# Kernel tuning notes

Hardware: AMD Instinct MI355X
Metric: run time of the kernel (lower is better)

Reference implementation:

```python
import jax, jax.numpy as jnp
import numpy as np

N, IN, H, C = 50000, 128, 256, 64
E_G, E_K = 600000, 800000
MLP_H = H // 2  # multiplier=2 (residual=False)
EPS = 1e-5


def _w(k, i, o):
    return (jax.random.normal(k, (i, o), jnp.float32) * np.float32(1.0 / np.sqrt(i)))


def setup_inputs() -> dict:
    key = jax.random.key(0)
    ks = jax.random.split(key, 32)
    inp = {
        "feat": jax.random.normal(ks[0], (N, IN), jnp.float32),
        "g_src": jax.random.randint(ks[1], (E_G,), 0, N, jnp.int32),
        "g_dst": jax.random.randint(ks[2], (E_G,), 0, N, jnp.int32),
        "k_src": jax.random.randint(ks[3], (E_K,), 0, N, jnp.int32),
        "k_dst": jax.random.randint(ks[4], (E_K,), 0, N, jnp.int32),
        # local GraphSAGE: 3 SAGEConv layers (IN->H, H->H, H->H)
        "lw_self_0": _w(ks[5], IN, H), "lw_neigh_0": _w(ks[6], IN, H), "lb_0": jnp.zeros((H,), jnp.float32),
        "lw_self_1": _w(ks[7], H, H),  "lw_neigh_1": _w(ks[8], H, H),  "lb_1": jnp.zeros((H,), jnp.float32),
        "lw_self_2": _w(ks[9], H, H),  "lw_neigh_2": _w(ks[10], H, H), "lb_2": jnp.zeros((H,), jnp.float32),
        # global GraphSAGE: 2 SAGEConv layers (IN->H, H->H)
        "gw_self_0": _w(ks[11], IN, H), "gw_neigh_0": _w(ks[12], IN, H), "gb_0": jnp.zeros((H,), jnp.float32),
        "gw_self_1": _w(ks[13], H, H),  "gw_neigh_1": _w(ks[14], H, H),  "gb_1": jnp.zeros((H,), jnp.float32),
        # MLP head: Linear(2H -> MLP_H), BatchNorm1d(MLP_H), ReLU, Linear(MLP_H -> C)
        "mlp_w1": _w(ks[15], 2 * H, MLP_H), "mlp_b1": jnp.zeros((MLP_H,), jnp.float32),
        "bn_gamma": jnp.ones((MLP_H,), jnp.float32), "bn_beta": jnp.zeros((MLP_H,), jnp.float32),
        "mlp_w2": _w(ks[16], MLP_H, C), "mlp_b2": jnp.zeros((C,), jnp.float32),
    }
    return inp


def sage_conv(src, dst, h, w_self, w_neigh, b):
    # DGL SAGEConv, mean aggregator: fc_self(h) + fc_neigh(mean_{u in N(v)} h_u) + bias
    msg = h[src]                                             # [E, d] irregular gather
    agg = jax.ops.segment_sum(msg, dst, num_segments=N)      # [N, d] irregular scatter-add
    deg = jax.ops.segment_sum(jnp.ones(src.shape, h.dtype), dst, num_segments=N)
    h_neigh = agg / jnp.maximum(deg, 1.0)[:, None]           # isolated nodes -> 0
    return h @ w_self + h_neigh @ w_neigh + b


def batch_norm(x, gamma, beta):
    mu = jnp.mean(x, axis=0)
    var = jnp.mean(jnp.square(x - mu), axis=0)  # biased var, as in torch BN forward
    return gamma * (x - mu) * jax.lax.rsqrt(var + EPS) + beta


def reference(feat, g_src, g_dst, k_src, k_dst,
              lw_self_0, lw_neigh_0, lb_0, lw_self_1, lw_neigh_1, lb_1,
              lw_self_2, lw_neigh_2, lb_2,
              gw_self_0, gw_neigh_0, gb_0, gw_self_1, gw_neigh_1, gb_1,
              mlp_w1, mlp_b1, bn_gamma, bn_beta, mlp_w2, mlp_b2):
    # local GraphSAGE (3 layers, relu between; dropout = identity in eval)
    h = feat
    h = jax.nn.relu(sage_conv(g_src, g_dst, h, lw_self_0, lw_neigh_0, lb_0))
    h = jax.nn.relu(sage_conv(g_src, g_dst, h, lw_self_1, lw_neigh_1, lb_1))
    local_emb = sage_conv(g_src, g_dst, h, lw_self_2, lw_neigh_2, lb_2)
    # global GraphSAGE on knn graph (2 layers)
    h = feat
    h = jax.nn.relu(sage_conv(k_src, k_dst, h, gw_self_0, gw_neigh_0, gb_0))
    global_emb = sage_conv(k_src, k_dst, h, gw_self_1, gw_neigh_1, gb_1)
    # fuse + BatchNorm-MLP head
    x = jnp.concatenate([local_emb, global_emb], axis=1)     # [N, 2H]
    x = x @ mlp_w1 + mlp_b1
    x = jax.nn.relu(batch_norm(x, bn_gamma, bn_beta))
    return x @ mlp_w2 + mlp_b2                               # [N, C]
```

## Files before the change

kernel.cpp:

```cpp
#include <hip/hip_runtime.h>

#define NN   50000
#define IN_F 128
#define HF   256
#define COUT 64
#define MLPH 128
#define EG   600000
#define EK   800000
#define RNG  6250
#define SUBR 1563
#define CAPG 80000
#define CAPK 106000
#define BN_EPS 1e-5f

typedef __attribute__((ext_vector_type(8))) short short8;
typedef __attribute__((ext_vector_type(8))) unsigned short ushort8;
typedef __attribute__((ext_vector_type(4))) float f32x4;

__device__ __forceinline__ unsigned short f2bf(float f) {
  union { float f; unsigned int u; } v; v.f = f;
  unsigned int r = v.u + 0x7FFFu + ((v.u >> 16) & 1u);
  return (unsigned short)(r >> 16);
}
__device__ __forceinline__ float bf2f(unsigned short s) {
  union { unsigned int u; float f; } v; v.u = ((unsigned int)s) << 16;
  return v.f;
}

__device__ __forceinline__ void gload_lds16(const void* g, void* l) {
  __builtin_amdgcn_global_load_lds((const __attribute__((address_space(1))) void*)g,
                                   (__attribute__((address_space(3))) void*)l, 16, 0, 0);
}

struct WDesc { const float* src; int rows; int cshift; int kofs; int ldk; int dofs; };
struct WPack { WDesc d[12]; };

__global__ __launch_bounds__(256) void prep_kernel(const float* __restrict__ feat,
                                                   unsigned short* __restrict__ featbf,
                                                   WPack p, unsigned short* __restrict__ wts) {
  int b = blockIdx.x;
  if (b < 3126) {
    int i = b * 256 + threadIdx.x;
    if (i < NN * IN_F / 8) {
      float4 a = *reinterpret_cast<const float4*>(&feat[i * 8]);
      float4 c = *reinterpret_cast<const float4*>(&feat[i * 8 + 4]);
      ushort8 o;
      o[0] = f2bf(a.x); o[1] = f2bf(a.y); o[2] = f2bf(a.z); o[3] = f2bf(a.w);
      o[4] = f2bf(c.x); o[5] = f2bf(c.y); o[6] = f2bf(c.z); o[7] = f2bf(c.w);
      *reinterpret_cast<ushort8*>(&featbf[i * 8]) = o;
    }
  } else {
    int wb = b - 3126;
    WDesc w = p.d[wb >> 5];
    int xb = wb & 31;
    int total = w.rows << w.cshift;
    int cmask = (1 << w.cshift) - 1;
    for (int idx = xb * 256 + threadIdx.x; idx < total; idx += 32 * 256) {
      int r = idx >> w.cshift, c = idx & cmask;
      wts[w.dofs + (size_t)c * w.ldk + w.kofs + r] = f2bf(w.src[idx]);
    }
  }
}

__global__ __launch_bounds__(128) void fuse_w_kernel(
    const float* __restrict__ wl2s, const float* __restrict__ wl2n,
    const float* __restrict__ wg1s, const float* __restrict__ wg1n,
    const float* __restrict__ w1, const float* __restrict__ bl2,
    const float* __restrict__ bg1, const float* __restrict__ b1,
    unsigned short* __restrict__ wf, float* __restrict__ bfused) {
  int b = blockIdx.x;
  int c = threadIdx.x;
  __shared__ float row[256];
  if (b < 1024) {
    int seg = b >> 8, i = b & 255;
    const float* W = (seg == 0) ? wl2s : (seg == 1) ? wl2n : (seg == 2) ? wg1s : wg1n;
    const float* w1b = w1 + ((seg < 2) ? 0 : 256) * MLPH;
    row[c] = W[i * 256 + c];
    row[c + 128] = W[i * 256 + 128 + c];
    __syncthreads();
    float acc = 0.f;
    for (int o = 0; o < 256; ++o) acc += row[o] * w1b[o * MLPH + c];
    unsigned short v = f2bf(acc);
    if (seg == 0)      wf[(size_t)c * 512 + i] = v;
    else if (seg == 2) wf[(size_t)c * 512 + 256 + i] = v;
    else if (seg == 1) wf[65536 + (size_t)c * 256 + i] = v;
    else               wf[98304 + (size_t)c * 256 + i] = v;
  } else {
    float acc = b1[c];
    for (int o = 0; o < 256; ++o) acc += bl2[o] * w1[o * MLPH + c];
    for (int o = 0; o < 256; ++o) acc += bg1[o] * w1[(256 + o) * MLPH + c];
    bfused[c] = acc;
  }
}

__global__ __launch_bounds__(256) void bucket_kernel(const int* __restrict__ g_src,
                                                     const int* __restrict__ g_dst,
                                                     const int* __restrict__ k_src,
                                                     const int* __restrict__ k_dst,
                                                     int* __restrict__ gcnt,
                                                     unsigned* __restrict__ bkt_g,
                                                     unsigned* __restrict__ bkt_k) {
  __shared__ unsigned buf[2048];
  __shared__ int rcnt[8], rbase[8], roff[8];
  const int gr = blockIdx.y;
  const int* src = gr ? k_src : g_src;
  const int* dst = gr ? k_dst : g_dst;
  unsigned* bkt = gr ? bkt_k : bkt_g;
  const int CAP = gr ? CAPK : CAPG;
  const int E = gr ? EK : EG;
  int* gc = gcnt + gr * 8;
  const int tid = threadIdx.x;
  const int e0 = blockIdx.x * 2048;
  if (e0 >= E) return;
  if (tid < 8) rcnt[tid] = 0;
  __syncthreads();
  unsigned vloc[8];
  int rloc[8], ploc[8];
#pragma unroll
  for (int i = 0; i < 8; ++i) {
    int e = e0 + i * 256 + tid;
    rloc[i] = -1;
    if (e < E) {
      int d = dst[e], s = src[e];
      int r = d / RNG;
      vloc[i] = ((unsigned)d << 16) | (unsigned)s;
      rloc[i] = r;
      ploc[i] = atomicAdd(&rcnt[r], 1);
    }
  }
  __syncthreads();
  if (tid == 0) {
    int acc = 0;
#pragma unroll
    for (int r = 0; r < 8; ++r) { roff[r] = acc; acc += rcnt[r]; }
  }
  __syncthreads();
#pragma unroll
  for (int i = 0; i < 8; ++i)
    if (rloc[i] >= 0) buf[roff[rloc[i]] + ploc[i]] = vloc[i];
  __syncthreads();
  if (tid < 8) rbase[tid] = atomicAdd(&gc[tid], rcnt[tid]);
  __syncthreads();
#pragma unroll
  for (int r = 0; r < 8; ++r) {
    int len = rcnt[r];
    unsigned* dstp = bkt + (size_t)r * CAP + rbase[r];
    for (int i = tid; i < len; i += 256) dstp[i] = buf[roff[r] + i];
  }
}

__global__ __launch_bounds__(256) void count_bucket(const unsigned* __restrict__ bkt_g,
                                                    const unsigned* __restrict__ bkt_k,
                                                    const int* __restrict__ gcnt,
                                                    int* __restrict__ cnt_g,
                                                    int* __restrict__ cnt_k, int CC) {
  __shared__ int hist[RNG];
  const int r = blockIdx.x, gr = blockIdx.y, z = blockIdx.z;
  const unsigned* b = (gr ? bkt_k : bkt_g) + (size_t)r * (gr ? CAPK : CAPG);
  int* cnt = gr ? cnt_k : cnt_g;
  const int n = gcnt[gr * 8 + r];
  const unsigned lo = r * RNG;
  for (int i = threadIdx.x; i < RNG; i += 256) hist[i] = 0;
  __syncthreads();
  for (int i = z * 256 + threadIdx.x; i < n; i += CC * 256) {
    unsigned d = (b[i] >> 16) - lo;
    atomicAdd(&hist[d], 1);
  }
  __syncthreads();
  for (int i = threadIdx.x; i < RNG; i += 256) {
    int v = hist[i];
    if (v) atomicAdd(&cnt[lo + i], v);
  }
}

__global__ __launch_bounds__(256) void scan_partial2(const int* __restrict__ cnt_g,
                                                     const int* __restrict__ cnt_k,
                                                     int* __restrict__ part, int n) {
  const int* cnt = blockIdx.y ? cnt_k : cnt_g;
  int* pp = part + blockIdx.y * 256;
  int i = blockIdx.x * 256 + threadIdx.x;
  int v = (i < n) ? cnt[i] : 0;
  __shared__ int ws[4];
  int lane = threadIdx.x & 63, wid = threadIdx.x >> 6;
  int x = v;
#pragma unroll
  for (int d = 1; d < 64; d <<= 1) { int y = __shfl_up(x, d, 64); if (lane >= d) x += y; }
  if (lane == 63) ws[wid] = x;
  __syncthreads();
  if (threadIdx.x == 0) pp[blockIdx.x] = ws[0] + ws[1] + ws[2] + ws[3];
}

__global__ __launch_bounds__(256) void scan_block2(int* __restrict__ part, int np) {
  int* pp = part + blockIdx.x * 256;
  __shared__ int ws[4];
  int tid = threadIdx.x, lane = tid & 63, wid = tid >> 6;
  int v = (tid < np) ? pp[tid] : 0;
  int x = v;
#pragma unroll
  for (int d = 1; d < 64; d <<= 1) { int y = __shfl_up(x, d, 64); if (lane >= d) x += y; }
  if (lane == 63) ws[wid] = x;
  __syncthreads();
  int add = 0;
#pragma unroll
  for (int k = 0; k < 4; ++k) if (k < wid) add += ws[k];
  if (tid < np) pp[tid] = x - v + add;
}

__global__ __launch_bounds__(256) void scan_final2(const int* __restrict__ cnt_g,
                                                   const int* __restrict__ cnt_k,
                                                   const int* __restrict__ part,
                                                   int* __restrict__ off_g,
                                                   int* __restrict__ off_k,
                                                   float* __restrict__ invg,
                                                   float* __restrict__ invk, int n) {
  const int* cnt = blockIdx.y ? cnt_k : cnt_g;
  const int* pp = part + blockIdx.y * 256;
  int* off = blockIdx.y ? off_k : off_g;
  float* inv = blockIdx.y ? invk : invg;
  int total = blockIdx.y ? EK : EG;
  int i = blockIdx.x * 256 + threadIdx.x;
  int v = (i < n) ? cnt[i] : 0;
  __shared__ int ws[4];
  int lane = threadIdx.x & 63, wid = threadIdx.x >> 6;
  int x = v;
#pragma unroll
  for (int d = 1; d < 64; d <<= 1) { int y = __shfl_up(x, d, 64); if (lane >= d) x += y; }
  if (lane == 63) ws[wid] = x;
  __syncthreads();
  int add = pp[blockIdx.x];
#pragma unroll
  for (int k = 0; k < 4; ++k) if (k < wid) add += ws[k];
  if (i < n) {
    off[i] = x - v + add;
    inv[i] = 1.0f / fmaxf((float)v, 1.0f);
  }
  if (i == 0) off[n] = total;
}

__global__ __launch_bounds__(1024) void fill_sub(const unsigned* __restrict__ bkt_g,
                                                 const unsigned* __restrict__ bkt_k,
                                                 const int* __restrict__ gcnt,
                                                 const int* __restrict__ off_g,
                                                 const int* __restrict__ off_k,
                                                 unsigned short* __restrict__ e16g,
                                                 unsigned short* __restrict__ e16k) {
  __shared__ int curs[SUBR];
  const int b = blockIdx.x;
  const int s = b & 3, r = (b >> 2) & 7, gr = b >> 5;
  const unsigned* bkt = (gr ? bkt_k : bkt_g) + (size_t)r * (gr ? CAPK : CAPG);
  const int* off = gr ? off_k : off_g;
  unsigned short* e16 = gr ? e16k : e16g;
  const int n = gcnt[gr * 8 + r];
  const int lo = r * RNG;
  const int slo = s * SUBR;
  int send = slo + SUBR;
  if (send > RNG) send = RNG;
  const int swid = send - slo;
  for (int i = threadIdx.x; i < swid; i += 1024) curs[i] = off[lo + slo + i];
  __syncthreads();
  for (int i = threadIdx.x; i < n; i += 1024) {
    unsigned v = bkt[i];
    int d = (int)(v >> 16) - lo - slo;
    if ((unsigned)d < (unsigned)swid) {
      int pz = atomicAdd(&curs[d], 1);
      e16[pz] = (unsigned short)(v & 0xffffu);
    }
  }
}

template <int DLOG2>
__global__ __launch_bounds__(256) void csr_aggregate(const unsigned short* __restrict__ h,
                                                     const int* __restrict__ off,
                                                     const unsigned short* __restrict__ esrc,
                                                     const float* __restrict__ inv,
                                                     unsigned short* __restrict__ out) {
  constexpr int TPN = (1 << DLOG2) / 8;
  constexpr int NPB = 256 / TPN;
  int node = blockIdx.x * NPB + ((int)threadIdx.x / TPN);
  int lane = threadIdx.x & (TPN - 1);
  if (node >= NN) return;
  int s = off[node], e = off[node + 1];
  float acc[8] = {0.f, 0.f, 0.f, 0.f, 0.f, 0.f, 0.f, 0.f};
  int j = s;
  for (; j + 3 < e; j += 4) {
    int s0 = esrc[j], s1 = esrc[j + 1], s2 = esrc[j + 2], s3 = esrc[j + 3];
    ushort8 v0 = *reinterpret_cast<const ushort8*>(&h[((size_t)s0 << DLOG2) + lane * 8]);
    ushort8 v1 = *reinterpret_cast<const ushort8*>(&h[((size_t)s1 << DLOG2) + lane * 8]);
    ushort8 v2 = *reinterpret_cast<const ushort8*>(&h[((size_t)s2 << DLOG2) + lane * 8]);
    ushort8 v3 = *reinterpret_cast<const ushort8*>(&h[((size_t)s3 << DLOG2) + lane * 8]);
#pragma unroll
    for (int i = 0; i < 8; ++i) acc[i] += bf2f(v0[i]);
#pragma unroll
    for (int i = 0; i < 8; ++i) acc[i] += bf2f(v1[i]);
#pragma unroll
    for (int i = 0; i < 8; ++i) acc[i] += bf2f(v2[i]);
#pragma unroll
    for (int i = 0; i < 8; ++i) acc[i] += bf2f(v3[i]);
  }
  for (; j < e; ++j) {
    int s0 = esrc[j];
    ushort8 v0 = *reinterpret_cast<const ushort8*>(&h[((size_t)s0 << DLOG2) + lane * 8]);
#pragma unroll
    for (int i = 0; i < 8; ++i) acc[i] += bf2f(v0[i]);
  }
  float sc = inv[node];
  ushort8 o;
#pragma unroll
  for (int i = 0; i < 8; ++i) o[i] = f2bf(acc[i] * sc);
  *reinterpret_cast<ushort8*>(&out[((size_t)node << DLOG2) + lane * 8]) = o;
}

template <int K1, int K2, bool RELU, bool OUT_BF16>
__global__ __launch_bounds__(256) void gemm_gl(
    const unsigned short* __restrict__ A1, const unsigned short* __restrict__ A2,
    const unsigned short* __restrict__ Bt, const float* __restrict__ bias,
    void* __restrict__ outv, int ldo, int nrows) {
  constexpr int KTOT = K1 + K2;
  constexpr int KT = KTOT / 64;
  __shared__ char smem[32768];
  unsigned short* sA = (unsigned short*)smem;
  unsigned short* sB = sA + 8192;

  const int t = threadIdx.x;
  const int lane = t & 63;
  const int w = t >> 6;
  const int wm = (w & 1) * 64, wn = (w >> 1) * 64;
  const int row0 = blockIdx.y * 128;
  const int n0 = blockIdx.x * 128;

  const int srow = (w << 5) + (lane >> 3);
  const int schunk = (lane & 7) << 3;

  f32x4 acc[4][4] = {};

  for (int kt = 0; kt < KT; ++kt) {
    const int kbase = kt * 64;
    const unsigned short* Asrc = (kbase < K1) ? A1 : A2;
    const int kA = (kbase < K1) ? kbase : (kbase - K1);
    const int lda = (kbase < K1) ? K1 : K2;
#pragma unroll
    for (int q = 0; q < 4; ++q) {
      int rA = srow + q * 8;
      int rowg = row0 + rA;
      if (rowg >= nrows) rowg = nrows - 1;
      gload_lds16(Asrc + (size_t)rowg * lda + kA + schunk,
                  sA + ((w << 5) + q * 8) * 64);
      gload_lds16(Bt + (size_t)(n0 + rA) * KTOT + kbase + schunk,
                  sB + ((w << 5) + q * 8) * 64);
    }
    __syncthreads();
#pragma unroll
    for (int kk = 0; kk < 2; ++kk) {
      const int ko = kk * 32 + (lane >> 4) * 8;
      short8 a[4], b[4];
#pragma unroll
      for (int mi = 0; mi < 4; ++mi)
        a[mi] = *reinterpret_cast<const short8*>(&sA[(wm + mi * 16 + (lane & 15)) * 64 + ko]);
#pragma unroll
      for (int ni = 0; ni < 4; ++ni)
        b[ni] = *reinterpret_cast<const short8*>(&sB[(wn + ni * 16 + (lane & 15)) * 64 + ko]);
#pragma unroll
      for (int mi = 0; mi < 4; ++mi)
#pragma unroll
        for (int ni = 0; ni < 4; ++ni)
          acc[mi][ni] = __builtin_amdgcn_mfma_f32_16x16x32_bf16(a[mi], b[ni], acc[mi][ni], 0, 0, 0);
    }
    __syncthreads();
  }

  float* Co = (float*)smem;
#pragma unroll
  for (int h = 0; h < 2; ++h) {
    __syncthreads();
    if ((w >> 1) == h) {
#pragma unroll
      for (int mi = 0; mi < 4; ++mi)
#pragma unroll
        for (int ni = 0; ni < 4; ++ni) {
          int col = ni * 16 + (lane & 15);
          int rowb = wm + mi * 16 + (lane >> 4) * 4;
#pragma unroll
          for (int j = 0; j < 4; ++j) Co[(rowb + j) * 64 + col] = acc[mi][ni][j];
        }
    }
    __syncthreads();
    int sr = t >> 1, cb = (t & 1) * 32;
    int r = row0 + sr;
    if (r < nrows) {
      float v[32];
#pragma unroll
      for (int i = 0; i < 32; ++i) {
        v[i] = Co[sr * 64 + cb + i] + bias[n0 + h * 64 + cb + i];
        if (RELU) v[i] = fmaxf(v[i], 0.f);
      }
      if (OUT_BF16) {
        unsigned short* dst = (unsigned short*)outv + (size_t)r * ldo + n0 + h * 64 + cb;
#pragma unroll
        for (int q = 0; q < 4; ++q) {
          ushort8 o;
#pragma unroll
          for (int i = 0; i < 8; ++i) o[i] = f2bf(v[q * 8 + i]);
          *reinterpret_cast<ushort8*>(dst + q * 8) = o;
        }
      } else {
        float* dst = (float*)outv + (size_t)r * ldo + n0 + h * 64 + cb;
#pragma unroll
        for (int q = 0; q < 8; ++q) {
          float4 o = make_float4(v[4 * q], v[4 * q + 1], v[4 * q + 2], v[4 * q + 3]);
          *reinterpret_cast<float4*>(dst + 4 * q) = o;
        }
      }
    }
  }
}

__global__ __launch_bounds__(256) void gemm_tail512(
    const unsigned short* __restrict__ A0, const unsigned short* __restrict__ A1,
    const unsigned short* __restrict__ Bt, const float* __restrict__ bias,
    const unsigned short* __restrict__ aYL, const unsigned short* __restrict__ aYG,
    float* __restrict__ outv, int nrows) {
  constexpr int KTOT = 512;
  constexpr int KT = 8;
  __shared__ char smem[32768];
  unsigned short* sA = (unsigned short*)smem;
  unsigned short* sB = sA + 8192;

  const int t = threadIdx.x;
  const int lane = t & 63;
  const int w = t >> 6;
  const int wm = (w & 1) * 64, wn = (w >> 1) * 64;
  const int row0 = blockIdx.y * 128;

  const int srow = (w << 5) + (lane >> 3);
  const int schunk = (lane & 7) << 3;

  f32x4 acc[4][4] = {};

  for (int kt = 0; kt < KT; ++kt) {
    const unsigned short* Asrc = (kt < 4) ? A0 : A1;
    const int kA = (kt & 3) * 64;
#pragma unroll
    for (int q = 0; q < 4; ++q) {
      int rA = srow + q * 8;
      int rowg = row0 + rA;
      if (rowg >= nrows) rowg = nrows - 1;
      gload_lds16(Asrc + (size_t)rowg * 256 + kA + schunk,
                  sA + ((w << 5) + q * 8) * 64);
      gload_lds16(Bt + (size_t)rA * KTOT + kt * 64 + schunk,
                  sB + ((w << 5) + q * 8) * 64);
    }
    __syncthreads();
#pragma unroll
    for (int kk = 0; kk < 2; ++kk) {
      const int ko = kk * 32 + (lane >> 4) * 8;
      short8 a[4], b[4];
#pragma unroll
      for (int mi = 0; mi < 4; ++mi)
        a[mi] = *reinterpret_cast<const short8*>(&sA[(wm + mi * 16 + (lane & 15)) * 64 + ko]);
#pragma unroll
      for (int ni = 0; ni < 4; ++ni)
        b[ni] = *reinterpret_cast<const short8*>(&sB[(wn + ni * 16 + (lane & 15)) * 64 + ko]);
#pragma unroll
      for (int mi = 0; mi < 4; ++mi)
#pragma unroll
        for (int ni = 0; ni < 4; ++ni)
          acc[mi][ni] = __builtin_amdgcn_mfma_f32_16x16x32_bf16(a[mi], b[ni], acc[mi][ni], 0, 0, 0);
    }
    __syncthreads();
  }

  float* Co = (float*)smem;
#pragma unroll
  for (int h = 0; h < 2; ++h) {
    __syncthreads();
    if ((w >> 1) == h) {
#pragma unroll
      for (int mi = 0; mi < 4; ++mi)
#pragma unroll
        for (int ni = 0; ni < 4; ++ni) {
          int col = ni * 16 + (lane & 15);
          int rowb = wm + mi * 16 + (lane >> 4) * 4;
#pragma unroll
          for (int j = 0; j < 4; ++j) Co[(rowb + j) * 64 + col] = acc[mi][ni][j];
        }
    }
    __syncthreads();
    int sr = t >> 1, cb = (t & 1) * 32;
    int r = row0 + sr;
    if (r < nrows) {
      float* dst = outv + (size_t)r * MLPH + h * 64 + cb;
#pragma unroll
      for (int q = 0; q < 4; ++q) {
        ushort8 ya = *reinterpret_cast<const ushort8*>(&aYL[(size_t)r * MLPH + h * 64 + cb + q * 8]);
        ushort8 yb = *reinterpret_cast<const ushort8*>(&aYG[(size_t)r * MLPH + h * 64 + cb + q * 8]);
        float v[8];
#pragma unroll
        for (int i = 0; i < 8; ++i)
          v[i] = Co[sr * 64 + cb + q * 8 + i] + bf2f(ya[i]) + bf2f(yb[i]) +
                 bias[h * 64 + cb + q * 8 + i];
        *reinterpret_cast<float4*>(dst + q * 8) = make_float4(v[0], v[1], v[2], v[3]);
        *reinterpret_cast<float4*>(dst + q * 8 + 4) = make_float4(v[4], v[5], v[6], v[7]);
      }
    }
  }
}

__global__ __launch_bounds__(256) void bn_stats_kernel(const float* __restrict__ x,
                                                       float* __restrict__ sums,
                                                       float* __restrict__ sumsq) {
  int c = threadIdx.x & 127;
  int rbase = (blockIdx.x * 256 + threadIdx.x) >> 7;
  int stride = (gridDim.x * 256) >> 7;
  float s = 0.f, s2 = 0.f;
  for (int r = rbase; r < NN; r += stride) {
    float v = x[(size_t)r * 128 + c];
    s += v;
    s2 += v * v;
  }
  __shared__ float ls[256], ls2[256];
  ls[threadIdx.x] = s;
  ls2[threadIdx.x] = s2;
  __syncthreads();
  if (threadIdx.x < 128) {
    s = ls[threadIdx.x] + ls[threadIdx.x + 128];
    s2 = ls2[threadIdx.x] + ls2[threadIdx.x + 128];
    atomicAdd(&sums[c], s);
    atomicAdd(&sumsq[c], s2);
  }
}

__global__ __launch_bounds__(128) void bn_finalize_kernel(float* __restrict__ stats,
                                                          const float* __restrict__ gamma,
                                                          const float* __restrict__ beta) {
  int c = threadIdx.x;
  float mu = stats[c] * (1.0f / NN);
  float var = stats[128 + c] * (1.0f / NN) - mu * mu;
  var = fmaxf(var, 0.f);
  float sc = gamma[c] * rsqrtf(var + BN_EPS);
  stats[256 + c] = sc;
  stats[384 + c] = beta[c] - mu * sc;
}

template <int K1, bool RELU>
__global__ __launch_bounds__(256) void gemm_mfma_bn(
    const float* __restrict__ A1v, const unsigned short* __restrict__ Bt,
    const float* __restrict__ bias, const float* __restrict__ bnscale,
    const float* __restrict__ bnshift, float* __restrict__ outv, int ldo, int nrows) {
  constexpr int KT = K1 / 64;
  constexpr int LDT = 72;
  __shared__ char smem[2 * 64 * LDT * 2];
  unsigned short* As = (unsigned short*)smem;
  unsigned short* Bs = As + 64 * LDT;
  float* Co = (float*)smem;
  constexpr int LDC = 68;

  const int t = threadIdx.x;
  const int lane = t & 63;
  const int w = t >> 6;
  const int wm = (w & 1) * 32, wn = (w >> 1) * 32;
  const int row0 = blockIdx.y * 64;
  const int n0 = blockIdx.x * 64;

  const int sr = t >> 2;
  const int skc = (t & 3) * 16;
  int rg = row0 + sr;
  if (rg >= nrows) rg = nrows - 1;

  f32x4 acc[2][2] = {};

  for (int kt = 0; kt < KT; ++kt) {
    const int kbase = kt * 64;
    {
      const float* xb = A1v + (size_t)rg * K1 + kbase + skc;
      ushort8 o0, o1;
#pragma unroll
      for (int i = 0; i < 8; ++i) {
        float v = xb[i] * bnscale[kbase + skc + i] + bnshift[kbase + skc + i];
        o0[i] = f2bf(fmaxf(v, 0.f));
      }
#pragma unroll
      for (int i = 0; i < 8; ++i) {
        float v = xb[8 + i] * bnscale[kbase + skc + 8 + i] + bnshift[kbase + skc + 8 + i];
        o1[i] = f2bf(fmaxf(v, 0.f));
      }
      *reinterpret_cast<ushort8*>(&As[sr * LDT + skc]) = o0;
      *reinterpret_cast<ushort8*>(&As[sr * LDT + skc + 8]) = o1;
    }
    {
      const unsigned short* bb = Bt + (size_t)(n0 + sr) * K1 + kbase + skc;
      int4 p0 = *reinterpret_cast<const int4*>(bb);
      int4 p1 = *reinterpret_cast<const int4*>(bb + 8);
      *reinterpret_cast<int4*>(&Bs[sr * LDT + skc]) = p0;
      *reinterpret_cast<int4*>(&Bs[sr * LDT + skc + 8]) = p1;
    }
    __syncthreads();
#pragma unroll
    for (int kk = 0; kk < 2; ++kk) {
      const int ko = kk * 32 + (lane >> 4) * 8;
      short8 a0 = *reinterpret_cast<const short8*>(&As[(wm + (lane & 15)) * LDT + ko]);
      short8 a1 = *reinterpret_cast<const short8*>(&As[(wm + 16 + (lane & 15)) * LDT + ko]);
      short8 b0 = *reinterpret_cast<const short8*>(&Bs[(wn + (lane & 15)) * LDT + ko]);
      short8 b1 = *reinterpret_cast<const short8*>(&Bs[(wn + 16 + (lane & 15)) * LDT + ko]);
      acc[0][0] = __builtin_amdgcn_mfma_f32_16x16x32_bf16(a0, b0, acc[0][0], 0, 0, 0);
      acc[0][1] = __builtin_amdgcn_mfma_f32_16x16x32_bf16(a0, b1, acc[0][1], 0, 0, 0);
      acc[1][0] = __builtin_amdgcn_mfma_f32_16x16x32_bf16(a1, b0, acc[1][0], 0, 0, 0);
      acc[1][1] = __builtin_amdgcn_mfma_f32_16x16x32_bf16(a1, b1, acc[1][1], 0, 0, 0);
    }
    __syncthreads();
  }

#pragma unroll
  for (int mi = 0; mi < 2; ++mi)
#pragma unroll
    for (int ni = 0; ni < 2; ++ni) {
      int col = wn + ni * 16 + (lane & 15);
      int rowb = wm + mi * 16 + (lane >> 4) * 4;
#pragma unroll
      for (int j = 0; j < 4; ++j) Co[(rowb + j) * LDC + col] = acc[mi][ni][j];
    }
  __syncthreads();
  {
    int r = row0 + sr;
    if (r < nrows) {
      float v[16];
#pragma unroll
      for (int i = 0; i < 16; ++i) {
        v[i] = Co[sr * LDC + skc + i] + bias[n0 + skc + i];
        if (RELU) v[i] = fmaxf(v[i], 0.f);
      }
      float* dst = outv + (size_t)r * ldo + n0 + skc;
#pragma unroll
      for (int i = 0; i < 4; ++i) {
        float4 o = make_float4(v[4 * i], v[4 * i + 1], v[4 * i + 2], v[4 * i + 3]);
        *reinterpret_cast<float4*>(dst + 4 * i) = o;
      }
    }
  }
}

extern "C" void kernel_launch(void* const* d_in, const int* in_sizes, int n_in,
                              void* d_out, int out_size, void* d_ws, size_t ws_size,
                              hipStream_t stream) {
  const float* feat = (const float*)d_in[0];
  const int* g_src = (const int*)d_in[1];
  const int* g_dst = (const int*)d_in[2];
  const int* k_src = (const int*)d_in[3];
  const int* k_dst = (const int*)d_in[4];
  const float* lb_0 = (const float*)d_in[7];
  const float* lb_1 = (const float*)d_in[10];
  const float* lb_2 = (const float*)d_in[13];
  const float* gb_0 = (const float*)d_in[16];
  const float* gb_1 = (const float*)d_in[19];
  const float* mlp_b1 = (const float*)d_in[21];
  const float* bn_gamma = (const float*)d_in[22];
  const float* bn_beta = (const float*)d_in[23];
  const float* mlp_b2 = (const float*)d_in[25];
  float* out = (float*)d_out;

  float* xf32 = (float*)d_ws;
  int* cnt_g = (int*)(xf32 + (size_t)NN * 128);
  int* cnt_k = cnt_g + NN;
  float* stats = (float*)(cnt_k + NN);
  int* gcnt = (int*)(stats + 512);
  float* zbias = (float*)(gcnt + 16);
  float* invg = zbias + 128;
  float* invk = invg + NN;
  int* off_g = (int*)(invk + NN);
  int* off_k = off_g + NN + 4;
  int* part = off_k + NN + 4;
  unsigned* bkt_g = (unsigned*)(part + 512);
  unsigned* bkt_k = bkt_g + 8 * CAPG;
  unsigned short* e16g = (unsigned short*)(bkt_k + 8 * CAPK);
  unsigned short* e16k = e16g + EG;
  unsigned short* featbf = e16k + EK;
  unsigned short* wts = featbf + (size_t)NN * IN_F;
  unsigned short* wf = wts + 598016;
  float* bfused = (float*)(wf + 131072);
  unsigned short* bfA = (unsigned short*)(bfused + 128);
  unsigned short* bfB = bfA + (size_t)NN * HF;
  unsigned short* bfAgg = bfB + (size_t)NN * HF;
  unsigned short* bfYL = bfAgg + (size_t)NN * HF;
  unsigned short* bfYG = bfYL + (size_t)NN * MLPH;
  unsigned short* bfAYL = bfYG + (size_t)NN * MLPH;
  unsigned short* bfAYG = bfAYL + (size_t)NN * MLPH;

  const int wL0 = 0, wL1 = 65536, wG0 = 327680, wH2 = 589824;
  const int wfYL = 65536, wfYG = 98304;

  dim3 blk(256);
  const int NB = (NN + 255) / 256;
  const int MB = (NN + 127) / 128;
  const dim3 gridH(2, MB);
  const dim3 gridM(1, MB);
  const int agg128_blocks = (NN + 15) / 16;
  const int agg256_blocks = (NN + 7) / 8;
  const int BKB = (EK + 2047) / 2048;
  const int CC = 8;

  hipMemsetAsync(cnt_g, 0,
                 (size_t)(2 * NN) * sizeof(int) + 512 * sizeof(float) + 16 * sizeof(int) +
                     128 * sizeof(float),
                 stream);

  WPack p;
  p.d[0] = {(const float*)d_in[5], 128, 8, 0, 256, wL0};
  p.d[1] = {(const float*)d_in[6], 128, 8, 128, 256, wL0};
  p.d[2] = {(const float*)d_in[8], 256, 8, 0, 512, wL1};
  p.d[3] = {(const float*)d_in[9], 256, 8, 256, 512, wL1};
  p.d[4] = {(const float*)d_in[11], 256, 8, 0, 512, 196608};
  p.d[5] = {(const float*)d_in[12], 256, 8, 256, 512, 196608};
  p.d[6] = {(const float*)d_in[14], 128, 8, 0, 256, wG0};
  p.d[7] = {(const float*)d_in[15], 128, 8, 128, 256, wG0};
  p.d[8] = {(const float*)d_in[17], 256, 8, 0, 512, 393216};
  p.d[9] = {(const float*)d_in[18], 256, 8, 256, 512, 393216};
  p.d[10] = {(const float*)d_in[20], 512, 7, 0, 512, 524288};
  p.d[11] = {(const float*)d_in[24], 128, 6, 0, 128, wH2};
  prep_kernel<<<3510, blk, 0, stream>>>(feat, featbf, p, wts);

  fuse_w_kernel<<<1025, 128, 0, stream>>>(
      (const float*)d_in[11], (const float*)d_in[12],
      (const float*)d_in[17], (const float*)d_in[18],
      (const float*)d_in[20], lb_2, gb_1, mlp_b1, wf, bfused);

  bucket_kernel<<<dim3(BKB, 2), blk, 0, stream>>>(g_src, g_dst, k_src, k_dst, gcnt, bkt_g, bkt_k);
  count_bucket<<<dim3(8, 2, CC), blk, 0, stream>>>(bkt_g, bkt_k, gcnt, cnt_g, cnt_k, CC);
  scan_partial2<<<dim3(NB, 2), blk, 0, stream>>>(cnt_g, cnt_k, part, NN);
  scan_block2<<<2, blk, 0, stream>>>(part, NB);
  scan_final2<<<dim3(NB, 2), blk, 0, stream>>>(cnt_g, cnt_k, part, off_g, off_k, invg, invk, NN);
  fill_sub<<<64, 1024, 0, stream>>>(bkt_g, bkt_k, gcnt, off_g, off_k, e16g, e16k);

  csr_aggregate<7><<<agg128_blocks, blk, 0, stream>>>(featbf, off_g, e16g, invg, bfAgg);
  gemm_gl<128, 128, true, true><<<gridH, blk, 0, stream>>>(
      featbf, bfAgg, wts + wL0, lb_0, bfA, HF, NN);
  csr_aggregate<8><<<agg256_blocks, blk, 0, stream>>>(bfA, off_g, e16g, invg, bfAgg);
  gemm_gl<256, 256, true, true><<<gridH, blk, 0, stream>>>(
      bfA, bfAgg, wts + wL1, lb_1, bfB, HF, NN);
  gemm_gl<256, 0, false, true><<<gridM, blk, 0, stream>>>(
      bfB, nullptr, wf + wfYL, zbias, bfYL, MLPH, NN);
  csr_aggregate<7><<<agg128_blocks, blk, 0, stream>>>(bfYL, off_g, e16g, invg, bfAYL);
  csr_aggregate<7><<<agg128_blocks, blk, 0, stream>>>(featbf, off_k, e16k, invk, bfAgg);
  gemm_gl<128, 128, true, true><<<gridH, blk, 0, stream>>>(
      featbf, bfAgg, wts + wG0, gb_0, bfA, HF, NN);
  gemm_gl<256, 0, false, true><<<gridM, blk, 0, stream>>>(
      bfA, nullptr, wf + wfYG, zbias, bfYG, MLPH, NN);
  csr_aggregate<7><<<agg128_blocks, blk, 0, stream>>>(bfYG, off_k, e16k, invk, bfAYG);

  gemm_tail512<<<gridM, blk, 0, stream>>>(bfB, bfA, wf, bfused, bfAYL, bfAYG, xf32, NN);

  bn_stats_kernel<<<256, blk, 0, stream>>>(xf32, stats, stats + 128);
  bn_finalize_kernel<<<1, 128, 0, stream>>>(stats, bn_gamma, bn_beta);

  gemm_mfma_bn<128, false><<<dim3(1, (NN + 63) / 64), blk, 0, stream>>>(
      xf32, wts + wH2, mlp_b2, stats + 256, stats + 384, out, COUT, NN);
}
```

Baseline: 486.8 us.

## Batch paired aggregations, fuse BN stats into tail GEMM, widen fill_sub split

Merges the two independent 128-wide aggregations (local/global input features, and YL/YG) into single two-plane launches, and reorders the schedule so both layer-0 GEMMs run back to back using separate buffers. BatchNorm column sums are now accumulated inside the tail GEMM epilogue via shared-memory partial sums and atomics, which removes a separate pass over the fp32 activations. fill_sub is split into 8 sub-ranges per bucket (128 blocks) for more parallelism, and the aggregation inner loop is unrolled to 8 gathers in flight. This adds extra buffer memory and more global atomics per block.

Result: faster. 461.2 us (-5.3%).

```diff
diff --git a/kernel.cpp b/kernel.cpp
--- a/kernel.cpp
+++ b/kernel.cpp
@@ -8,7 +8,7 @@
 #define EG   600000
 #define EK   800000
 #define RNG  6250
-#define SUBR 1563
+#define SUBR 782
 #define CAPG 80000
 #define CAPK 106000
 #define BN_EPS 1e-5f
@@ -246,7 +246,7 @@
                                                  unsigned short* __restrict__ e16k) {
   __shared__ int curs[SUBR];
   const int b = blockIdx.x;
-  const int s = b & 3, r = (b >> 2) & 7, gr = b >> 5;
+  const int s = b & 7, r = (b >> 3) & 7, gr = b >> 6;
   const unsigned* bkt = (gr ? bkt_k : bkt_g) + (size_t)r * (gr ? CAPK : CAPG);
   const int* off = gr ? off_k : off_g;
   unsigned short* e16 = gr ? e16k : e16g;
@@ -256,6 +256,7 @@
   int send = slo + SUBR;
   if (send > RNG) send = RNG;
   const int swid = send - slo;
+  if (swid <= 0) return;
   for (int i = threadIdx.x; i < swid; i += 1024) curs[i] = off[lo + slo + i];
   __syncthreads();
   for (int i = threadIdx.x; i < n; i += 1024) {
@@ -266,6 +267,53 @@
       e16[pz] = (unsigned short)(v & 0xffffu);
     }
   }
+}
+
+template <int DLOG2>
+__device__ __forceinline__ void agg_node(const unsigned short* __restrict__ h,
+                                         const int* __restrict__ off,
+                                         const unsigned short* __restrict__ esrc,
+                                         const float* __restrict__ inv,
+                                         unsigned short* __restrict__ out,
+                                         int node, int lane) {
+  int s = off[node], e = off[node + 1];
+  float acc[8] = {0.f, 0.f, 0.f, 0.f, 0.f, 0.f, 0.f, 0.f};
+  int j = s;
+  for (; j + 7 < e; j += 8) {
+    ushort8 v[8];
+#pragma unroll
+    for (int q = 0; q < 8; ++q) {
+      int sq = esrc[j + q];
+      v[q] = *reinterpret_cast<const ushort8*>(&h[((size_t)sq << DLOG2) + lane * 8]);
+    }
+#pragma unroll
+    for (int q = 0; q < 8; ++q)
+#pragma unroll
+      for (int i = 0; i < 8; ++i) acc[i] += bf2f(v[q][i]);
+  }
+  for (; j + 3 < e; j += 4) {
+    ushort8 v[4];
+#pragma unroll
+    for (int q = 0; q < 4; ++q) {
+      int sq = esrc[j + q];
+      v[q] = *reinterpret_cast<const ushort8*>(&h[((size_t)sq << DLOG2) + lane * 8]);
+    }
+#pragma unroll
+    for (int q = 0; q < 4; ++q)
+#pragma unroll
+      for (int i = 0; i < 8; ++i) acc[i] += bf2f(v[q][i]);
+  }
+  for (; j < e; ++j) {
+    int s0 = esrc[j];
+    ushort8 v0 = *reinterpret_cast<const ushort8*>(&h[((size_t)s0 << DLOG2) + lane * 8]);
+#pragma unroll
+    for (int i = 0; i < 8; ++i) acc[i] += bf2f(v0[i]);
+  }
+  float sc = inv[node];
+  ushort8 o;
+#pragma unroll
+  for (int i = 0; i < 8; ++i) o[i] = f2bf(acc[i] * sc);
+  *reinterpret_cast<ushort8*>(&out[((size_t)node << DLOG2) + lane * 8]) = o;
 }
 
 template <int DLOG2>
@@ -279,35 +327,24 @@
   int node = blockIdx.x * NPB + ((int)threadIdx.x / TPN);
   int lane = threadIdx.x & (TPN - 1);
   if (node >= NN) return;
-  int s = off[node], e = off[node + 1];
-  float acc[8] = {0.f, 0.f, 0.f, 0.f, 0.f, 0.f, 0.f, 0.f};
-  int j = s;
-  for (; j + 3 < e; j += 4) {
-    int s0 = esrc[j], s1 = esrc[j + 1], s2 = esrc[j + 2], s3 = esrc[j + 3];
-    ushort8 v0 = *reinterpret_cast<const ushort8*>(&h[((size_t)s0 << DLOG2) + lane * 8]);
-    ushort8 v1 = *reinterpret_cast<const ushort8*>(&h[((size_t)s1 << DLOG2) + lane * 8]);
-    ushort8 v2 = *reinterpret_cast<const ushort8*>(&h[((size_t)s2 << DLOG2) + lane * 8]);
-    ushort8 v3 = *reinterpret_cast<const ushort8*>(&h[((size_t)s3 << DLOG2) + lane * 8]);
-#pragma unroll
-    for (int i = 0; i < 8; ++i) acc[i] += bf2f(v0[i]);
-#pragma unroll
-    for (int i = 0; i < 8; ++i) acc[i] += bf2f(v1[i]);
-#pragma unroll
-    for (int i = 0; i < 8; ++i) acc[i] += bf2f(v2[i]);
-#pragma unroll
-    for (int i = 0; i < 8; ++i) acc[i] += bf2f(v3[i]);
-  }
-  for (; j < e; ++j) {
-    int s0 = esrc[j];
-    ushort8 v0 = *reinterpret_cast<const ushort8*>(&h[((size_t)s0 << DLOG2) + lane * 8]);
-#pragma unroll
-    for (int i = 0; i < 8; ++i) acc[i] += bf2f(v0[i]);
-  }
-  float sc = inv[node];
-  ushort8 o;
-#pragma unroll
-  for (int i = 0; i < 8; ++i) o[i] = f2bf(acc[i] * sc);
-  *reinterpret_cast<ushort8*>(&out[((size_t)node << DLOG2) + lane * 8]) = o;
+  agg_node<DLOG2>(h, off, esrc, inv, out, node, lane);
+}
+
+__global__ __launch_bounds__(256) void csr_aggregate2(
+    const unsigned short* __restrict__ h0, const int* __restrict__ off0,
+    const unsigned short* __restrict__ e0, const float* __restrict__ inv0,
+    unsigned short* __restrict__ out0,
+    const unsigned short* __restrict__ h1, const int* __restrict__ off1,
+    const unsigned short* __restrict__ e1, const float* __restrict__ inv1,
+    unsigned short* __restrict__ out1) {
+  constexpr int TPN = 16, NPB = 16;
+  int node = blockIdx.x * NPB + ((int)threadIdx.x / TPN);
+  int lane = threadIdx.x & (TPN - 1);
+  if (node >= NN) return;
+  if (blockIdx.y == 0)
+    agg_node<7>(h0, off0, e0, inv0, out0, node, lane);
+  else
+    agg_node<7>(h1, off1, e1, inv1, out1, node, lane);
 }
 
 template <int K1, int K2, bool RELU, bool OUT_BF16>
@@ -418,10 +455,11 @@
     const unsigned short* __restrict__ A0, const unsigned short* __restrict__ A1,
     const unsigned short* __restrict__ Bt, const float* __restrict__ bias,
     const unsigned short* __restrict__ aYL, const unsigned short* __restrict__ aYG,
-    float* __restrict__ outv, int nrows) {
+    float* __restrict__ outv, float* __restrict__ bnsums, int nrows) {
   constexpr int KTOT = 512;
   constexpr int KT = 8;
   __shared__ char smem[32768];
+  __shared__ float psum[4][64], psum2[4][64];
   unsigned short* sA = (unsigned short*)smem;
   unsigned short* sB = sA + 8192;
 
@@ -495,37 +533,38 @@
         ushort8 yb = *reinterpret_cast<const ushort8*>(&aYG[(size_t)r * MLPH + h * 64 + cb + q * 8]);
         float v[8];
 #pragma unroll
-        for (int i = 0; i < 8; ++i)
+        for (int i = 0; i < 8; ++i) {
           v[i] = Co[sr * 64 + cb + q * 8 + i] + bf2f(ya[i]) + bf2f(yb[i]) +
                  bias[h * 64 + cb + q * 8 + i];
+          Co[sr * 64 + cb + q * 8 + i] = v[i];
+        }
         *reinterpret_cast<float4*>(dst + q * 8) = make_float4(v[0], v[1], v[2], v[3]);
         *reinterpret_cast<float4*>(dst + q * 8 + 4) = make_float4(v[4], v[5], v[6], v[7]);
       }
     }
-  }
-}
-
-__global__ __launch_bounds__(256) void bn_stats_kernel(const float* __restrict__ x,
-                                                       float* __restrict__ sums,
-                                                       float* __restrict__ sumsq) {
-  int c = threadIdx.x & 127;
-  int rbase = (blockIdx.x * 256 + threadIdx.x) >> 7;
-  int stride = (gridDim.x * 256) >> 7;
-  float s = 0.f, s2 = 0.f;
-  for (int r = rbase; r < NN; r += stride) {
-    float v = x[(size_t)r * 128 + c];
-    s += v;
-    s2 += v * v;
-  }
-  __shared__ float ls[256], ls2[256];
-  ls[threadIdx.x] = s;
-  ls2[threadIdx.x] = s2;
-  __syncthreads();
-  if (threadIdx.x < 128) {
-    s = ls[threadIdx.x] + ls[threadIdx.x + 128];
-    s2 = ls2[threadIdx.x] + ls2[threadIdx.x + 128];
-    atomicAdd(&sums[c], s);
-    atomicAdd(&sumsq[c], s2);
+    __syncthreads();
+    {
+      int c = t & 63, rq = t >> 6;
+      float s = 0.f, s2 = 0.f;
+      int rbeg = rq * 32;
+      for (int rr = rbeg; rr < rbeg + 32; ++rr) {
+        if (row0 + rr < nrows) {
+          float v = Co[rr * 64 + c];
+          s += v;
+          s2 += v * v;
+        }
+      }
+      psum[rq][c] = s;
+      psum2[rq][c] = s2;
+    }
+    __syncthreads();
+    if (t < 64) {
+      float s = psum[0][t] + psum[1][t] + psum[2][t] + psum[3][t];
+      float s2 = psum2[0][t] + psum2[1][t] + psum2[2][t] + psum2[3][t];
+      atomicAdd(&bnsums[h * 64 + t], s);
+      atomicAdd(&bnsums[128 + h * 64 + t], s2);
+    }
+    __syncthreads();
   }
 }
 
@@ -676,10 +715,13 @@
   unsigned short* wts = featbf + (size_t)NN * IN_F;
   unsigned short* wf = wts + 598016;
   float* bfused = (float*)(wf + 131072);
-  unsigned short* bfA = (unsigned short*)(bfused + 128);
-  unsigned short* bfB = bfA + (size_t)NN * HF;
-  unsigned short* bfAgg = bfB + (size_t)NN * HF;
-  unsigned short* bfYL = bfAgg + (size_t)NN * HF;
+  unsigned short* hL0 = (unsigned short*)(bfused + 128);
+  unsigned short* hG0 = hL0 + (size_t)NN * HF;
+  unsigned short* hL1 = hG0 + (size_t)NN * HF;
+  unsigned short* aggT = hL1 + (size_t)NN * HF;
+  unsigned short* aggFG = aggT + (size_t)NN * HF;
+  unsigned short* aggFK = aggFG + (size_t)NN * MLPH;
+  unsigned short* bfYL = aggFK + (size_t)NN * MLPH;
   unsigned short* bfYG = bfYL + (size_t)NN * MLPH;
   unsigned short* bfAYL = bfYG + (size_t)NN * MLPH;
   unsigned short* bfAYG = bfAYL + (size_t)NN * MLPH;
@@ -727,29 +769,27 @@
   scan_partial2<<<dim3(NB, 2), blk, 0, stream>>>(cnt_g, cnt_k, part, NN);
   scan_block2<<<2, blk, 0, stream>>>(part, NB);
   scan_final2<<<dim3(NB, 2), blk, 0, stream>>>(cnt_g, cnt_k, part, off_g, off_k, invg, invk, NN);
-  fill_sub<<<64, 1024, 0, stream>>>(bkt_g, bkt_k, gcnt, off_g, off_k, e16g, e16k);
-
-  csr_aggregate<7><<<agg128_blocks, blk, 0, stream>>>(featbf, off_g, e16g, invg, bfAgg);
+  fill_sub<<<128, 1024, 0, stream>>>(bkt_g, bkt_k, gcnt, off_g, off_k, e16g, e16k);
+
+  csr_aggregate2<<<dim3(agg128_blocks, 2), blk, 0, stream>>>(
+      featbf, off_g, e16g, invg, aggFG, featbf, off_k, e16k, invk, aggFK);
   gemm_gl<128, 128, true, true><<<gridH, blk, 0, stream>>>(
-      featbf, bfAgg, wts + wL0, lb_0, bfA, HF, NN);
-  csr_aggregate<8><<<agg256_blocks, blk, 0, stream>>>(bfA, off_g, e16g, invg, bfAgg);
+      featbf, aggFG, wts + wL0, lb_0, hL0, HF, NN);
+  gemm_gl<128, 128, true, true><<<gridH, blk, 0, stream>>>(
+      featbf, aggFK, wts + wG0, gb_0, hG0, HF, NN);
+  csr_aggregate<8><<<agg256_blocks, blk, 0, stream>>>(hL0, off_g, e16g, invg, aggT);
   gemm_gl<256, 256, true, true><<<gridH, blk, 0, stream>>>(
-      bfA, bfAgg, wts + wL1, lb_1, bfB, HF, NN);
+      hL0, aggT, wts + wL1, lb_1, hL1, HF, NN);
   gemm_gl<256, 0, false, true><<<gridM, blk, 0, stream>>>(
-      bfB, nullptr, wf + wfYL, zbias, bfYL, MLPH, NN);
-  csr_aggregate<7><<<agg128_blocks, blk, 0, stream>>>(bfYL, off_g, e16g, invg, bfAYL);
-  csr_aggregate<7><<<agg128_blocks, blk, 0, stream>>>(featbf, off_k, e16k, invk, bfAgg);
-  gemm_gl<128, 128, true, true><<<gridH, blk, 0, stream>>>(
-      featbf, bfAgg, wts + wG0, gb_0, bfA, HF, NN);
+      hL1, nullptr, wf + wfYL, zbias, bfYL, MLPH, NN);
   gemm_gl<256, 0, false, true><<<gridM, blk, 0, stream>>>(
-      bfA, nullptr, wf + wfYG, zbias, bfYG, MLPH, NN);
-  csr_aggregate<7><<<agg128_blocks, blk, 0, stream>>>(bfYG, off_k, e16k, invk, bfAYG);
-
-  gemm_tail512<<<gridM, blk, 0, stream>>>(bfB, bfA, wf, bfused, bfAYL, bfAYG, xf32, NN);
-
-  bn_stats_kernel<<<256, blk, 0, stream>>>(xf32, stats, stats + 128);
+      hG0, nullptr, wf + wfYG, zbias, bfYG, MLPH, NN);
+  csr_aggregate2<<<dim3(agg128_blocks, 2), blk, 0, stream>>>(
+      bfYL, off_g, e16g, invg, bfAYL, bfYG, off_k, e16k, invk, bfAYG);
+
+  gemm_tail512<<<gridM, blk, 0, stream>>>(hL1, hG0, wf, bfused, bfAYL, bfAYG, xf32, stats, NN);
+
   bn_finalize_kernel<<<1, 128, 0, stream>>>(stats, bn_gamma, bn_beta);
-
   gemm_mfma_bn<128, false><<<dim3(1, (NN + 63) / 64), blk, 0, stream>>>(
       xf32, wts + wH2, mlp_b2, stats + 256, stats + 384, out, COUT, NN);
 }
```
